# Kernel optimization log

Measured on AMD Instinct MI355X. Metric: run time of the kernel, lower is better.

## Reference

```python
import jax, jax.numpy as jnp
import numpy as np

B, L, D = 8, 2048, 2048
NH, HD = 32, 64          # num_heads, head_dim (D = NH*HD)
CS = 16                  # inner_net_chunk_size
BASE_LR = 1.0            # inner-loop base learning rate
EPS = 1e-6
ROPE_BASE = 10000.0


def setup_inputs() -> dict:
    key = jax.random.key(0)
    ks = jax.random.split(key, 6)
    s = 0.02
    return {
        "hidden_states": jax.random.normal(ks[0], (B, L, D), jnp.float32),
        "wq": jax.random.normal(ks[1], (D, D), jnp.float32) * s,
        "wk": jax.random.normal(ks[2], (D, D), jnp.float32) * s,
        "wv": jax.random.normal(ks[3], (D, D), jnp.float32) * s,
        "wo": jax.random.normal(ks[4], (D, D), jnp.float32) * s,
        "W1": jax.random.normal(ks[5], (NH, HD, HD), jnp.float32) * s,
        "b1": jnp.zeros((NH, 1, HD), jnp.float32),
        "ttt_norm_weight": jnp.ones((NH, HD), jnp.float32),
        "ttt_norm_bias": jnp.zeros((NH, HD), jnp.float32),
    }


def _rotate_half(x):
    x1, x2 = jnp.split(x, 2, axis=-1)
    return jnp.concatenate((-x2, x1), axis=-1)


def _permute_qk(x):
    b, h, l, f = x.shape
    return x.reshape(b, h, l, f // 2, 2).transpose(0, 1, 2, 4, 3).reshape(b, h, l, f)


def _undo_permute_qk(x):
    b, h, l, f = x.shape
    return x.reshape(b, h, l, 2, f // 2).transpose(0, 1, 2, 4, 3).reshape(b, h, l, f)


def _ln_fwd(x, g, b):
    mu = x.mean(-1, keepdims=True)
    var = ((x - mu) ** 2).mean(-1, keepdims=True)
    xh = (x - mu) * jax.lax.rsqrt(var + EPS)
    return g * xh + b


def _ln_fused_l2_bwd(x, target, g, b):
    # grad of 0.5*||LN(x) - target||^2 w.r.t. x, fused (TTT inner-loop loss grad)
    f = x.shape[-1]
    mu = x.mean(-1, keepdims=True)
    var = ((x - mu) ** 2).mean(-1, keepdims=True)
    std = jnp.sqrt(var + EPS)
    xh = (x - mu) / std
    gout = (g * xh + b) - target
    gxh = gout * g
    return (f * gxh - gxh.sum(-1, keepdims=True)
            - xh * (gxh * xh).sum(-1, keepdims=True)) / (f * std)


def reference(hidden_states, wq, wk, wv, wo, W1, b1, ttt_norm_weight, ttt_norm_bias):
    Bx, Lx, Dx = hidden_states.shape
    nc = Lx // CS

    def proj(w):  # [B,L,D] -> [B,NH,L,HD]
        return (hidden_states @ w).reshape(Bx, Lx, NH, HD).transpose(0, 2, 1, 3)

    XQ, XK, XV = proj(wq), proj(wk), proj(wv)

    # rotary embedding (with permute/undo as in the source)
    inv_freq = 1.0 / (ROPE_BASE ** (jnp.arange(0, HD, 2, dtype=jnp.float32) / HD))
    freqs = jnp.outer(jnp.arange(Lx, dtype=jnp.float32), inv_freq)
    emb = jnp.concatenate((freqs, freqs), axis=-1)
    cos, sin = jnp.cos(emb)[None, None], jnp.sin(emb)[None, None]
    XQ, XK = _permute_qk(XQ), _permute_qk(XK)
    XQ = XQ * cos + _rotate_half(XQ) * sin
    XK = XK * cos + _rotate_half(XK) * sin
    XQ, XK = _undo_permute_qk(XQ), _undo_permute_qk(XK)

    def chunk(x):  # [B,NH,L,HD] -> [nc,B,NH,CS,HD]
        return x.reshape(Bx, NH, nc, CS, HD).transpose(2, 0, 1, 3, 4)

    XQc, XKc, XVc = chunk(XQ), chunk(XK), chunk(XV)

    g = ttt_norm_weight[None, :, None, :]   # [1,NH,1,HD]
    bb = ttt_norm_bias[None, :, None, :]

    token_idx = 1.0 / jnp.arange(1, CS + 1, dtype=jnp.float32)   # buffer from __init__
    eta = BASE_LR * token_idx                                    # [CS]
    tril_eta = jnp.tril(jnp.ones((CS, CS), jnp.float32)) * eta[:, None]
    last_eta = eta[-1]

    W1_0 = jnp.broadcast_to(W1[None], (Bx, NH, HD, HD))
    b1_0 = jnp.broadcast_to(b1[None], (Bx, NH, 1, HD))

    def step(carry, xs):
        W1s, b1s = carry
        xq, xk, xv = xs                                          # [B,NH,CS,HD]
        Z1 = jnp.einsum('bhkf,bhfg->bhkg', xk, W1s) + b1s
        grad = _ln_fused_l2_bwd(Z1, xv - xk, g, bb)              # dl/dZ1
        attn = jnp.tril(jnp.einsum('bhkf,bhlf->bhkl', xq, xk))   # causal within chunk
        b1_bar = b1s - jnp.einsum('kl,bhlf->bhkf', tril_eta, grad)
        Z1_bar = (jnp.einsum('bhkf,bhfg->bhkg', xq, W1s)
                  - jnp.einsum('bhkl,bhlf->bhkf', eta[None, None, :, None] * attn, grad)
                  + b1_bar)
        W1_new = W1s - last_eta * jnp.einsum('bhkf,bhkg->bhfg', xk, grad)
        b1_new = b1s - last_eta * grad.sum(-2, keepdims=True)
        out = xq + _ln_fwd(Z1_bar, g, bb)                        # residual + post-LN
        return (W1_new, b1_new), out

    _, outs = jax.lax.scan(step, (W1_0, b1_0), (XQc, XKc, XVc))  # [nc,B,NH,CS,HD]
    out = (outs.transpose(1, 2, 0, 3, 4).reshape(Bx, NH, Lx, HD)
               .transpose(0, 2, 1, 3).reshape(Bx, Lx, Dx))
    return out @ wo
```

## Files before the change

kernel.cpp:

```cpp
#include <hip/hip_runtime.h>

typedef __bf16 bf16;
typedef __bf16 bf16x4 __attribute__((ext_vector_type(4)));
typedef __bf16 bf16x8 __attribute__((ext_vector_type(8)));
typedef float floatx4 __attribute__((ext_vector_type(4)));

#define BB 8
#define LL 2048
#define DD 2048
#define NHH 32
#define HDD 64

#define MFMA16(a, b, c) __builtin_amdgcn_mfma_f32_16x16x32_bf16(a, b, c, 0, 0, 0)

__device__ __forceinline__ void gl_lds16(const void* g, void* l) {
  __builtin_amdgcn_global_load_lds((const __attribute__((address_space(1))) void*)g,
                                   (__attribute__((address_space(3))) void*)l, 16, 0, 0);
}

__global__ __launch_bounds__(256) void cast_bf16(const float* __restrict__ src,
                                                 bf16* __restrict__ dst)
{
  size_t i = ((size_t)blockIdx.x * 256 + threadIdx.x) * 8;
  floatx4 a = *(const floatx4*)(src + i);
  floatx4 b = *(const floatx4*)(src + i + 4);
  bf16x8 v;
  v[0] = (bf16)a[0]; v[1] = (bf16)a[1]; v[2] = (bf16)a[2]; v[3] = (bf16)a[3];
  v[4] = (bf16)b[0]; v[5] = (bf16)b[1]; v[6] = (bf16)b[2]; v[7] = (bf16)b[3];
  *(bf16x8*)(dst + i) = v;
}

__global__ __launch_bounds__(256) void transpose1(const float* __restrict__ src,
                                                  bf16* __restrict__ dst)
{
  __shared__ float tile[64][65];
  const int t = threadIdx.x;
  const int col = t & 63, rw = t >> 6;
  const int bx = blockIdx.x * 64, by = blockIdx.y * 64;
  for (int i = rw; i < 64; i += 4)
    tile[i][col] = src[(size_t)(by + i) * DD + bx + col];
  __syncthreads();
  for (int i = rw; i < 64; i += 4)
    dst[(size_t)(bx + i) * DD + by + col] = (bf16)tile[col][i];
}

template<int AIDX, int EPI>
__global__ __launch_bounds__(256) void gemm_bt(const bf16* __restrict__ Ab,
    const bf16* __restrict__ BT, void* __restrict__ Cv)
{
  constexpr int Kd = 2048;
  __shared__ alignas(16) bf16 As[128 * 64];
  __shared__ alignas(16) bf16 Bs[128 * 64];
  const int t = threadIdx.x;
  const int id = blockIdx.y * 16 + blockIdx.x;
  const int swz = (id & 7) * 256 + (id >> 3);
  const int bn = swz & 15, bm = swz >> 4;
  const int wave = t >> 6, lane = t & 63;
  const int m16 = lane & 15, quad = lane >> 4;
  floatx4 acc[2][8] = {};
  const int r0 = t >> 3;
  const int scc = (t & 7) ^ (r0 & 7);
  const bf16* Bb = BT + (size_t)(bn * 128) * Kd;
  char* AsB = (char*)As + wave * 1024;
  char* BsB = (char*)Bs + wave * 1024;

  for (int k0 = 0; k0 < Kd; k0 += 64) {
    for (int i = 0; i < 4; ++i) {
      int r = r0 + 32 * i;
      int col = k0 + scc * 8;
      const bf16* ga;
      if (AIDX == 0) {
        ga = Ab + (size_t)(bm * 128 + r) * Kd + col;
      } else {
        int R = bm * 128 + r;
        int b = R >> 11, l = R & 2047;
        int h = col >> 6, f = col & 63;
        ga = Ab + (((size_t)(b * NHH + h) * LL + l) * HDD + f);
      }
      gl_lds16(ga, AsB + i * 4096);
      gl_lds16(Bb + (size_t)r * Kd + col, BsB + i * 4096);
    }
    __syncthreads();
    const int sw = m16 & 7;
    for (int kk = 0; kk < 2; ++kk) {
      bf16x8 af[2], bfr[8];
      const int c = ((kk * 4 + quad) ^ sw) * 8;
      for (int mt = 0; mt < 2; ++mt)
        af[mt] = *(const bf16x8*)&As[(wave * 32 + mt * 16 + m16) * 64 + c];
      for (int nt = 0; nt < 8; ++nt)
        bfr[nt] = *(const bf16x8*)&Bs[(nt * 16 + m16) * 64 + c];
      for (int mt = 0; mt < 2; ++mt)
        for (int nt = 0; nt < 8; ++nt)
          acc[mt][nt] = MFMA16(af[mt], bfr[nt], acc[mt][nt]);
    }
    __syncthreads();
  }

  for (int mt = 0; mt < 2; ++mt)
    for (int nt = 0; nt < 8; ++nt)
      for (int rg = 0; rg < 4; ++rg) {
        int row = bm * 128 + wave * 32 + mt * 16 + quad * 4 + rg;
        int col = bn * 128 + nt * 16 + m16;
        if (EPI == 0) {
          ((float*)Cv)[(size_t)row * DD + col] = acc[mt][nt][rg];
        } else {
          int b = row >> 11, l = row & 2047;
          int h = col >> 6, f = col & 63;
          ((bf16*)Cv)[((size_t)(b * NHH + h) * LL + l) * HDD + f] = (bf16)acc[mt][nt][rg];
        }
      }
}

__global__ __launch_bounds__(256) void rope_qk(bf16* __restrict__ Q, bf16* __restrict__ Kt)
{
  bf16* X = blockIdx.y ? Kt : Q;
  unsigned p = blockIdx.x * 256u + threadIdx.x;
  int i = p & 31;
  int l = (p >> 5) & 2047;
  int bh = p >> 16;
  float invf = expf(-(float)i * 0.28782313662425573f);
  float th = (float)l * invf;
  float cs = cosf(th), sn = sinf(th);
  size_t off = (size_t)bh * (LL * HDD) + (size_t)l * HDD + 2 * i;
  float x0 = (float)X[off], x1 = (float)X[off + 1];
  X[off]     = (bf16)(x0 * cs - x1 * sn);
  X[off + 1] = (bf16)(x1 * cs + x0 * sn);
}

__global__ __launch_bounds__(256) void ttt_scan(
    const bf16* Q, const bf16* __restrict__ Kx,
    const bf16* __restrict__ V, const float* __restrict__ W1g,
    const float* __restrict__ b1g, const float* __restrict__ gw,
    const float* __restrict__ gb, bf16* O)
{
  const int bh = blockIdx.x, h = bh & 31;
  const int t = threadIdx.x;
  const int wave = t >> 6, lane = t & 63;
  const int q = lane >> 4, i16 = lane & 15;
  const int kr = t >> 4, sr = t & 15, f0 = sr * 4;

  __shared__ alignas(16) bf16 W1Th[64 * 72];
  __shared__ alignas(16) bf16 W1Tl[64 * 72];
  __shared__ alignas(16) bf16 xqs[2][16 * 72];
  __shared__ alignas(16) bf16 xks[2][16 * 72];
  __shared__ alignas(16) bf16 xvs[2][16 * 72];
  __shared__ alignas(16) bf16 xkTs[64 * 24];
  __shared__ alignas(16) bf16 gTh[64 * 24];
  __shared__ alignas(16) bf16 gTl[64 * 24];
  __shared__ alignas(16) bf16 Pm[16 * 24];
  __shared__ alignas(16) float Z1s[16 * 68];

  floatx4 accW[4];
  const float* Wg = W1g + (size_t)h * 4096;
  for (int mt = 0; mt < 4; ++mt)
    for (int r = 0; r < 4; ++r)
      accW[mt][r] = Wg[(16 * mt + 4 * q + r) * 64 + 16 * wave + i16];
  float b1r = b1g[h * 64 + 16 * wave + i16];

  for (int mt = 0; mt < 4; ++mt) {
    bf16x4 h4, l4;
    for (int r = 0; r < 4; ++r) {
      float w = accW[mt][r];
      bf16 hi = (bf16)w;
      h4[r] = hi; l4[r] = (bf16)(w - (float)hi);
    }
    int base = (16 * wave + i16) * 72 + 16 * mt + 4 * q;
    *(bf16x4*)&W1Th[base] = h4;
    *(bf16x4*)&W1Tl[base] = l4;
  }

  float gq[4], bq[4];
  for (int j = 0; j < 4; ++j) {
    gq[j] = gw[h * 64 + f0 + j];
    bq[j] = gb[h * 64 + f0 + j];
  }
  float etar[4];
  for (int r = 0; r < 4; ++r) etar[r] = 1.0f / (float)(4 * q + r + 1);

  const size_t qbase = (size_t)bh * (LL * HDD);
  bf16x4 rq = *(const bf16x4*)(Q  + qbase + kr * 64 + f0);
  bf16x4 rk = *(const bf16x4*)(Kx + qbase + kr * 64 + f0);
  bf16x4 rv = *(const bf16x4*)(V  + qbase + kr * 64 + f0);

  for (int c = 0; c < 128; ++c) {
    const int pb = c & 1;
    *(bf16x4*)&xqs[pb][kr * 72 + f0] = rq;
    *(bf16x4*)&xks[pb][kr * 72 + f0] = rk;
    *(bf16x4*)&xvs[pb][kr * 72 + f0] = rv;
    for (int j = 0; j < 4; ++j)
      xkTs[(f0 + j) * 24 + kr] = (bf16)((float)rk[j] * -0.0625f);
    __syncthreads();

    bf16x8 akf[2], whi[2], wlo[2];
    akf[0] = *(const bf16x8*)&xks[pb][i16 * 72 + q * 8];
    akf[1] = *(const bf16x8*)&xks[pb][i16 * 72 + 32 + q * 8];
    {
      int wb = (16 * wave + i16) * 72 + q * 8;
      whi[0] = *(const bf16x8*)&W1Th[wb];
      whi[1] = *(const bf16x8*)&W1Th[wb + 32];
      wlo[0] = *(const bf16x8*)&W1Tl[wb];
      wlo[1] = *(const bf16x8*)&W1Tl[wb + 32];
    }
    {
      floatx4 z = {b1r, b1r, b1r, b1r};
      z = MFMA16(akf[0], whi[0], z);
      z = MFMA16(akf[1], whi[1], z);
      z = MFMA16(akf[0], wlo[0], z);
      z = MFMA16(akf[1], wlo[1], z);
      for (int r = 0; r < 4; ++r)
        Z1s[(4 * q + r) * 68 + 16 * wave + i16] = z[r];
    }
    if (wave == 0) {
      bf16x8 aq0 = *(const bf16x8*)&xqs[pb][i16 * 72 + q * 8];
      bf16x8 aq1 = *(const bf16x8*)&xqs[pb][i16 * 72 + 32 + q * 8];
      floatx4 at = {};
      at = MFMA16(aq0, akf[0], at);
      at = MFMA16(aq1, akf[1], at);
      for (int r = 0; r < 4; ++r) {
        int krow = 4 * q + r;
        float pv = (i16 <= krow) ? -(at[r] + 1.0f) * etar[r] : 0.0f;
        Pm[krow * 24 + i16] = (bf16)pv;
      }
    }
    __syncthreads();

    {
      floatx4 z4 = *(const floatx4*)&Z1s[kr * 68 + f0];
      float tg[4], sum = 0.f, ssq = 0.f;
      for (int j = 0; j < 4; ++j) {
        tg[j] = (float)rv[j] - (float)rk[j];
        sum += z4[j]; ssq += z4[j] * z4[j];
      }
      for (int m = 1; m < 16; m <<= 1) { sum += __shfl_xor(sum, m, 64); ssq += __shfl_xor(ssq, m, 64); }
      float mu = sum * (1.f / 64.f);
      float var = ssq * (1.f / 64.f) - mu * mu;
      float rstd = rsqrtf(var + 1e-6f);
      float xh[4], gx[4], s1 = 0.f, s2 = 0.f;
      for (int j = 0; j < 4; ++j) {
        xh[j] = (z4[j] - mu) * rstd;
        float go = gq[j] * xh[j] + bq[j] - tg[j];
        gx[j] = go * gq[j];
        s1 += gx[j]; s2 += gx[j] * xh[j];
      }
      for (int m = 1; m < 16; m <<= 1) { s1 += __shfl_xor(s1, m, 64); s2 += __shfl_xor(s2, m, 64); }
      for (int j = 0; j < 4; ++j) {
        float gr = (64.f * gx[j] - s1 - xh[j] * s2) * (rstd * (1.f / 64.f));
        bf16 hi = (bf16)gr;
        gTh[(f0 + j) * 24 + kr] = hi;
        gTl[(f0 + j) * 24 + kr] = (bf16)(gr - (float)hi);
      }
    }
    __syncthreads();

    {
      const size_t cb = qbase + (size_t)(c + 1) * 1024 + kr * 64 + f0;
      rq = *(const bf16x4*)(Q  + cb);
      rk = *(const bf16x4*)(Kx + cb);
      rv = *(const bf16x4*)(V  + cb);
    }

    {
      bf16x8 aq0 = *(const bf16x8*)&xqs[pb][i16 * 72 + q * 8];
      bf16x8 aq1 = *(const bf16x8*)&xqs[pb][i16 * 72 + 32 + q * 8];
      bf16x8 pf  = *(const bf16x8*)&Pm[i16 * 24 + (q & 1) * 8];
      const bf16* gT = (q < 2) ? gTh : gTl;
      bf16x8 bgp = *(const bf16x8*)&gT[(16 * wave + i16) * 24 + (q & 1) * 8];
      floatx4 zb = {b1r, b1r, b1r, b1r};
      zb = MFMA16(aq0, whi[0], zb);
      zb = MFMA16(aq1, whi[1], zb);
      zb = MFMA16(aq0, wlo[0], zb);
      zb = MFMA16(aq1, wlo[1], zb);
      zb = MFMA16(pf, bgp, zb);
      for (int r = 0; r < 4; ++r)
        Z1s[(4 * q + r) * 68 + 16 * wave + i16] = zb[r];

      for (int mt = 0; mt < 4; ++mt) {
        bf16x8 axk = *(const bf16x8*)&xkTs[(16 * mt + i16) * 24 + (q & 1) * 8];
        accW[mt] = MFMA16(axk, bgp, accW[mt]);
      }
      for (int mt = 0; mt < 4; ++mt) {
        bf16x4 h4, l4;
        for (int r = 0; r < 4; ++r) {
          float w = accW[mt][r];
          bf16 hi = (bf16)w;
          h4[r] = hi; l4[r] = (bf16)(w - (float)hi);
        }
        int base = (16 * wave + i16) * 72 + 16 * mt + 4 * q;
        *(bf16x4*)&W1Th[base] = h4;
        *(bf16x4*)&W1Tl[base] = l4;
      }
      {
        const bf16* rh = &gTh[(16 * wave + i16) * 24];
        const bf16* rl = &gTl[(16 * wave + i16) * 24];
        bf16x8 a0 = *(const bf16x8*)rh, a1 = *(const bf16x8*)(rh + 8);
        bf16x8 a2 = *(const bf16x8*)rl, a3 = *(const bf16x8*)(rl + 8);
        float s = 0.f;
        for (int j = 0; j < 8; ++j)
          s += (float)a0[j] + (float)a1[j] + (float)a2[j] + (float)a3[j];
        b1r -= 0.0625f * s;
      }
    }
    __syncthreads();

    {
      floatx4 z4 = *(const floatx4*)&Z1s[kr * 68 + f0];
      float sum = 0.f, ssq = 0.f;
      for (int j = 0; j < 4; ++j) { sum += z4[j]; ssq += z4[j] * z4[j]; }
      for (int m = 1; m < 16; m <<= 1) { sum += __shfl_xor(sum, m, 64); ssq += __shfl_xor(ssq, m, 64); }
      float mu = sum * (1.f / 64.f);
      float var = ssq * (1.f / 64.f) - mu * mu;
      float rstd = rsqrtf(var + 1e-6f);
      bf16x4 xq4 = *(const bf16x4*)&xqs[pb][kr * 72 + f0];
      bf16x4 o4;
      for (int j = 0; j < 4; ++j)
        o4[j] = (bf16)((float)xq4[j] + gq[j] * ((z4[j] - mu) * rstd) + bq[j]);
      *(bf16x4*)(O + qbase + (size_t)c * 1024 + kr * 64 + f0) = o4;
    }
  }
}

extern "C" void kernel_launch(void* const* d_in, const int* in_sizes, int n_in,
                              void* d_out, int out_size, void* d_ws, size_t ws_size,
                              hipStream_t stream)
{
  const float* X  = (const float*)d_in[0];
  const float* wq = (const float*)d_in[1];
  const float* wk = (const float*)d_in[2];
  const float* wv = (const float*)d_in[3];
  const float* wo = (const float*)d_in[4];
  const float* W1 = (const float*)d_in[5];
  const float* b1 = (const float*)d_in[6];
  const float* gw = (const float*)d_in[7];
  const float* gb = (const float*)d_in[8];

  bf16* ws = (bf16*)d_ws;
  const size_t NEl = (size_t)BB * LL * DD;
  bf16* Qb = ws;
  bf16* Kb = ws + NEl;
  bf16* WT = ws + 2 * NEl;
  bf16* Vb = (bf16*)d_out;
  bf16* Xb = (bf16*)d_out + NEl;

  cast_bf16<<<dim3(16384), 256, 0, stream>>>(X, Xb);
  transpose1<<<dim3(32, 32), 256, 0, stream>>>(wq, WT);
  gemm_bt<0, 1><<<dim3(16, 128), 256, 0, stream>>>(Xb, WT, Qb);
  transpose1<<<dim3(32, 32), 256, 0, stream>>>(wk, WT);
  gemm_bt<0, 1><<<dim3(16, 128), 256, 0, stream>>>(Xb, WT, Kb);
  transpose1<<<dim3(32, 32), 256, 0, stream>>>(wv, WT);
  gemm_bt<0, 1><<<dim3(16, 128), 256, 0, stream>>>(Xb, WT, Vb);
  rope_qk<<<dim3(65536, 2), 256, 0, stream>>>(Qb, Kb);
  ttt_scan<<<dim3(256), 256, 0, stream>>>(Qb, Kb, Vb, W1, b1, gw, gb, Qb);
  transpose1<<<dim3(32, 32), 256, 0, stream>>>(wo, WT);
  gemm_bt<1, 0><<<dim3(16, 128), 256, 0, stream>>>(Qb, WT, d_out);
}
```

Baseline: 1.209 ms.

## Fuse RoPE into QK projection epilogue and stream scan inputs via registers

Removes the standalone rotary kernel by applying the rotation inside the Q/K GEMM epilogue, using a lane shuffle to get the paired element and fast sincos. The TTT scan kernel now loads MFMA operand fragments for Q and K directly from global memory into registers and prefetches the next chunk, dropping the shared-memory staging buffers. Z1 scratch is double-buffered instead of the Q/K/V tiles. This cuts a full extra read/write pass over Q and K and trims syncs in the serial scan, at the cost of fast-math trig precision for large positions.

```diff
diff --git a/kernel.cpp b/kernel.cpp
--- a/kernel.cpp
+++ b/kernel.cpp
@@ -44,7 +44,7 @@
     dst[(size_t)(bx + i) * DD + by + col] = (bf16)tile[col][i];
 }
 
-template<int AIDX, int EPI>
+template<int AIDX, int EPI, int RP>
 __global__ __launch_bounds__(256) void gemm_bt(const bf16* __restrict__ Ab,
     const bf16* __restrict__ BT, void* __restrict__ Cv)
 {
@@ -96,35 +96,36 @@
     __syncthreads();
   }
 
+  float invf[8];
+  if (RP) {
+#pragma unroll
+    for (int nt = 0; nt < 8; ++nt) {
+      int col = bn * 128 + nt * 16 + m16;
+      int i = (col >> 1) & 31;
+      invf[nt] = __expf(-(float)i * 0.28782313662425573f);
+    }
+  }
+
   for (int mt = 0; mt < 2; ++mt)
     for (int nt = 0; nt < 8; ++nt)
       for (int rg = 0; rg < 4; ++rg) {
         int row = bm * 128 + wave * 32 + mt * 16 + quad * 4 + rg;
         int col = bn * 128 + nt * 16 + m16;
+        float v = acc[mt][nt][rg];
+        if (RP) {
+          float o = __shfl_xor(v, 1, 64);
+          float sn, cs;
+          __sincosf((float)(row & 2047) * invf[nt], &sn, &cs);
+          v = (m16 & 1) ? (v * cs + o * sn) : (v * cs - o * sn);
+        }
         if (EPI == 0) {
-          ((float*)Cv)[(size_t)row * DD + col] = acc[mt][nt][rg];
+          ((float*)Cv)[(size_t)row * DD + col] = v;
         } else {
           int b = row >> 11, l = row & 2047;
           int h = col >> 6, f = col & 63;
-          ((bf16*)Cv)[((size_t)(b * NHH + h) * LL + l) * HDD + f] = (bf16)acc[mt][nt][rg];
+          ((bf16*)Cv)[((size_t)(b * NHH + h) * LL + l) * HDD + f] = (bf16)v;
         }
       }
-}
-
-__global__ __launch_bounds__(256) void rope_qk(bf16* __restrict__ Q, bf16* __restrict__ Kt)
-{
-  bf16* X = blockIdx.y ? Kt : Q;
-  unsigned p = blockIdx.x * 256u + threadIdx.x;
-  int i = p & 31;
-  int l = (p >> 5) & 2047;
-  int bh = p >> 16;
-  float invf = expf(-(float)i * 0.28782313662425573f);
-  float th = (float)l * invf;
-  float cs = cosf(th), sn = sinf(th);
-  size_t off = (size_t)bh * (LL * HDD) + (size_t)l * HDD + 2 * i;
-  float x0 = (float)X[off], x1 = (float)X[off + 1];
-  X[off]     = (bf16)(x0 * cs - x1 * sn);
-  X[off + 1] = (bf16)(x1 * cs + x0 * sn);
 }
 
 __global__ __launch_bounds__(256) void ttt_scan(
@@ -141,14 +142,11 @@
 
   __shared__ alignas(16) bf16 W1Th[64 * 72];
   __shared__ alignas(16) bf16 W1Tl[64 * 72];
-  __shared__ alignas(16) bf16 xqs[2][16 * 72];
-  __shared__ alignas(16) bf16 xks[2][16 * 72];
-  __shared__ alignas(16) bf16 xvs[2][16 * 72];
   __shared__ alignas(16) bf16 xkTs[64 * 24];
   __shared__ alignas(16) bf16 gTh[64 * 24];
   __shared__ alignas(16) bf16 gTl[64 * 24];
   __shared__ alignas(16) bf16 Pm[16 * 24];
-  __shared__ alignas(16) float Z1s[16 * 68];
+  __shared__ alignas(16) float Z1s[2][16 * 68];
 
   floatx4 accW[4];
   const float* Wg = W1g + (size_t)h * 4096;
@@ -178,22 +176,25 @@
   for (int r = 0; r < 4; ++r) etar[r] = 1.0f / (float)(4 * q + r + 1);
 
   const size_t qbase = (size_t)bh * (LL * HDD);
-  bf16x4 rq = *(const bf16x4*)(Q  + qbase + kr * 64 + f0);
-  bf16x4 rk = *(const bf16x4*)(Kx + qbase + kr * 64 + f0);
-  bf16x4 rv = *(const bf16x4*)(V  + qbase + kr * 64 + f0);
+  const int foff = i16 * 64 + q * 8;
+  const int poff = kr * 64 + f0;
+
+  bf16x8 ak0 = *(const bf16x8*)(Kx + qbase + foff);
+  bf16x8 ak1 = *(const bf16x8*)(Kx + qbase + foff + 32);
+  bf16x8 aq0 = *(const bf16x8*)(Q  + qbase + foff);
+  bf16x8 aq1 = *(const bf16x8*)(Q  + qbase + foff + 32);
+  bf16x4 rq = *(const bf16x4*)(Q  + qbase + poff);
+  bf16x4 rk = *(const bf16x4*)(Kx + qbase + poff);
+  bf16x4 rv = *(const bf16x4*)(V  + qbase + poff);
+
+  __syncthreads();
 
   for (int c = 0; c < 128; ++c) {
     const int pb = c & 1;
-    *(bf16x4*)&xqs[pb][kr * 72 + f0] = rq;
-    *(bf16x4*)&xks[pb][kr * 72 + f0] = rk;
-    *(bf16x4*)&xvs[pb][kr * 72 + f0] = rv;
     for (int j = 0; j < 4; ++j)
       xkTs[(f0 + j) * 24 + kr] = (bf16)((float)rk[j] * -0.0625f);
-    __syncthreads();
-
-    bf16x8 akf[2], whi[2], wlo[2];
-    akf[0] = *(const bf16x8*)&xks[pb][i16 * 72 + q * 8];
-    akf[1] = *(const bf16x8*)&xks[pb][i16 * 72 + 32 + q * 8];
+
+    bf16x8 whi[2], wlo[2];
     {
       int wb = (16 * wave + i16) * 72 + q * 8;
       whi[0] = *(const bf16x8*)&W1Th[wb];
@@ -203,19 +204,17 @@
     }
     {
       floatx4 z = {b1r, b1r, b1r, b1r};
-      z = MFMA16(akf[0], whi[0], z);
-      z = MFMA16(akf[1], whi[1], z);
-      z = MFMA16(akf[0], wlo[0], z);
-      z = MFMA16(akf[1], wlo[1], z);
+      z = MFMA16(ak0, whi[0], z);
+      z = MFMA16(ak1, whi[1], z);
+      z = MFMA16(ak0, wlo[0], z);
+      z = MFMA16(ak1, wlo[1], z);
       for (int r = 0; r < 4; ++r)
-        Z1s[(4 * q + r) * 68 + 16 * wave + i16] = z[r];
+        Z1s[pb][(4 * q + r) * 68 + 16 * wave + i16] = z[r];
     }
     if (wave == 0) {
-      bf16x8 aq0 = *(const bf16x8*)&xqs[pb][i16 * 72 + q * 8];
-      bf16x8 aq1 = *(const bf16x8*)&xqs[pb][i16 * 72 + 32 + q * 8];
       floatx4 at = {};
-      at = MFMA16(aq0, akf[0], at);
-      at = MFMA16(aq1, akf[1], at);
+      at = MFMA16(aq0, ak0, at);
+      at = MFMA16(aq1, ak1, at);
       for (int r = 0; r < 4; ++r) {
         int krow = 4 * q + r;
         float pv = (i16 <= krow) ? -(at[r] + 1.0f) * etar[r] : 0.0f;
@@ -225,7 +224,7 @@
     __syncthreads();
 
     {
-      floatx4 z4 = *(const floatx4*)&Z1s[kr * 68 + f0];
+      floatx4 z4 = *(const floatx4*)&Z1s[pb][kr * 68 + f0];
       float tg[4], sum = 0.f, ssq = 0.f;
       for (int j = 0; j < 4; ++j) {
         tg[j] = (float)rv[j] - (float)rk[j];
@@ -252,16 +251,16 @@
     }
     __syncthreads();
 
-    {
-      const size_t cb = qbase + (size_t)(c + 1) * 1024 + kr * 64 + f0;
-      rq = *(const bf16x4*)(Q  + cb);
-      rk = *(const bf16x4*)(Kx + cb);
-      rv = *(const bf16x4*)(V  + cb);
-    }
-
-    {
-      bf16x8 aq0 = *(const bf16x8*)&xqs[pb][i16 * 72 + q * 8];
-      bf16x8 aq1 = *(const bf16x8*)&xqs[pb][i16 * 72 + 32 + q * 8];
+    const size_t nb = qbase + (size_t)(c + 1) * 1024;
+    bf16x8 nak0 = *(const bf16x8*)(Kx + nb + foff);
+    bf16x8 nak1 = *(const bf16x8*)(Kx + nb + foff + 32);
+    bf16x8 naq0 = *(const bf16x8*)(Q  + nb + foff);
+    bf16x8 naq1 = *(const bf16x8*)(Q  + nb + foff + 32);
+    bf16x4 nrq = *(const bf16x4*)(Q  + nb + poff);
+    bf16x4 nrk = *(const bf16x4*)(Kx + nb + poff);
+    bf16x4 nrv = *(const bf16x4*)(V  + nb + poff);
+
+    {
       bf16x8 pf  = *(const bf16x8*)&Pm[i16 * 24 + (q & 1) * 8];
       const bf16* gT = (q < 2) ? gTh : gTl;
       bf16x8 bgp = *(const bf16x8*)&gT[(16 * wave + i16) * 24 + (q & 1) * 8];
@@ -272,7 +271,7 @@
       zb = MFMA16(aq1, wlo[1], zb);
       zb = MFMA16(pf, bgp, zb);
       for (int r = 0; r < 4; ++r)
-        Z1s[(4 * q + r) * 68 + 16 * wave + i16] = zb[r];
+        Z1s[pb][(4 * q + r) * 68 + 16 * wave + i16] = zb[r];
 
       for (int mt = 0; mt < 4; ++mt) {
         bf16x8 axk = *(const bf16x8*)&xkTs[(16 * mt + i16) * 24 + (q & 1) * 8];
@@ -303,19 +302,20 @@
     __syncthreads();
 
     {
-      floatx4 z4 = *(const floatx4*)&Z1s[kr * 68 + f0];
+      floatx4 z4 = *(const floatx4*)&Z1s[pb][kr * 68 + f0];
       float sum = 0.f, ssq = 0.f;
       for (int j = 0; j < 4; ++j) { sum += z4[j]; ssq += z4[j] * z4[j]; }
       for (int m = 1; m < 16; m <<= 1) { sum += __shfl_xor(sum, m, 64); ssq += __shfl_xor(ssq, m, 64); }
       float mu = sum * (1.f / 64.f);
       float var = ssq * (1.f / 64.f) - mu * mu;
       float rstd = rsqrtf(var + 1e-6f);
-      bf16x4 xq4 = *(const bf16x4*)&xqs[pb][kr * 72 + f0];
       bf16x4 o4;
       for (int j = 0; j < 4; ++j)
-        o4[j] = (bf16)((float)xq4[j] + gq[j] * ((z4[j] - mu) * rstd) + bq[j]);
-      *(bf16x4*)(O + qbase + (size_t)c * 1024 + kr * 64 + f0) = o4;
-    }
+        o4[j] = (bf16)((float)rq[j] + gq[j] * ((z4[j] - mu) * rstd) + bq[j]);
+      *(bf16x4*)(O + qbase + (size_t)c * 1024 + poff) = o4;
+    }
+    ak0 = nak0; ak1 = nak1; aq0 = naq0; aq1 = naq1;
+    rq = nrq; rk = nrk; rv = nrv;
   }
 }
 
@@ -343,13 +343,12 @@
 
   cast_bf16<<<dim3(16384), 256, 0, stream>>>(X, Xb);
   transpose1<<<dim3(32, 32), 256, 0, stream>>>(wq, WT);
-  gemm_bt<0, 1><<<dim3(16, 128), 256, 0, stream>>>(Xb, WT, Qb);
+  gemm_bt<0, 1, 1><<<dim3(16, 128), 256, 0, stream>>>(Xb, WT, Qb);
   transpose1<<<dim3(32, 32), 256, 0, stream>>>(wk, WT);
-  gemm_bt<0, 1><<<dim3(16, 128), 256, 0, stream>>>(Xb, WT, Kb);
+  gemm_bt<0, 1, 1><<<dim3(16, 128), 256, 0, stream>>>(Xb, WT, Kb);
   transpose1<<<dim3(32, 32), 256, 0, stream>>>(wv, WT);
-  gemm_bt<0, 1><<<dim3(16, 128), 256, 0, stream>>>(Xb, WT, Vb);
-  rope_qk<<<dim3(65536, 2), 256, 0, stream>>>(Qb, Kb);
+  gemm_bt<0, 1, 0><<<dim3(16, 128), 256, 0, stream>>>(Xb, WT, Vb);
   ttt_scan<<<dim3(256), 256, 0, stream>>>(Qb, Kb, Vb, W1, b1, gw, gb, Qb);
   transpose1<<<dim3(32, 32), 256, 0, stream>>>(wo, WT);
-  gemm_bt<1, 0><<<dim3(16, 128), 256, 0, stream>>>(Qb, WT, d_out);
-}
+  gemm_bt<1, 0, 0><<<dim3(16, 128), 256, 0, stream>>>(Qb, WT, d_out);
+}
```

Result: no change. 1.202 ms (-0.6%).
